# Kernel tuning notes

Measured on AMD Instinct MI355X. Metric: run time of the kernel, lower is better.

Reference implementation:

```python
import jax, jax.numpy as jnp
import numpy as np

NUM_HEADS = 8
TOP_K = 2
ROUTER_EPS = 1e-5
LN_EPS = 1e-5
ROPE_BASE = 10000.0


def _layernorm(x, g, b):
    m = x.mean(-1, keepdims=True)
    v = ((x - m) ** 2).mean(-1, keepdims=True)
    return (x - m) * jax.lax.rsqrt(v + LN_EPS) * g + b


def _rope_tables(frames, height, width, head_dim, dtype):
    # dim split per axis; head_dim divisible by 3 with even parts (96 -> 32/32/32)
    dpa = head_dim // 3

    def freqs(n, d):
        inv = 1.0 / (ROPE_BASE ** (jnp.arange(0, d, 2, dtype=jnp.float32) / d))
        f = jnp.outer(jnp.arange(n, dtype=jnp.float32), inv)
        return jnp.concatenate([f, f], axis=-1)  # [n, d]

    fx, fy, ft = freqs(width, dpa), freqs(height, dpa), freqs(frames, dpa)

    def grid(ax, ay, at):
        gx = jnp.broadcast_to(ax[None, None, :, :], (frames, height, width, dpa))
        gy = jnp.broadcast_to(ay[None, :, None, :], (frames, height, width, dpa))
        gt = jnp.broadcast_to(at[:, None, None, :], (frames, height, width, dpa))
        return jnp.concatenate([gx, gy, gt], -1).reshape(frames * height * width, 3 * dpa)

    cos = grid(jnp.cos(fx), jnp.cos(fy), jnp.cos(ft)).astype(dtype)
    sin = grid(jnp.sin(fx), jnp.sin(fy), jnp.sin(ft)).astype(dtype)
    return cos, sin


def _apply_rope(x, cos, sin):
    # x: [B, H, S, hd]; cos/sin: [S, hd] (broadcast over B, H)
    h = x.shape[-1] // 2
    rot = jnp.concatenate([-x[..., h:], x[..., :h]], axis=-1)
    return x * cos + rot * sin


def _expert(x, g, u, d):
    # SwiGLU expert: down(silu(gate(x)) * up(x))
    return (jax.nn.silu(x @ g) * (x @ u)) @ d


def _block(x, cos, sin, ln1_g, ln1_b, w_qkv, w_out, gate_w,
           eg, eu, ed, sg, su, sd, ln2_g, ln2_b):
    B, S, D = x.shape
    hd = D // NUM_HEADS
    # --- 3D-RoPE attention (pre-LN, non-causal) ---
    xn = _layernorm(x, ln1_g, ln1_b)
    qkv = (xn @ w_qkv).reshape(B, S, 3, NUM_HEADS, hd)
    q = jnp.moveaxis(qkv[:, :, 0], 1, 2)  # [B, H, S, hd]
    k = jnp.moveaxis(qkv[:, :, 1], 1, 2)
    v = jnp.moveaxis(qkv[:, :, 2], 1, 2)
    q = _apply_rope(q, cos, sin)
    k = _apply_rope(k, cos, sin)
    scores = jnp.einsum('bhqd,bhkd->bhqk', q, k) * (hd ** -0.5)
    attn = jax.nn.softmax(scores, axis=-1)
    o = jnp.einsum('bhqk,bhkd->bhqd', attn, v)
    o = jnp.moveaxis(o, 1, 2).reshape(B, S, D) @ w_out
    x = x + o
    # --- temporal MoE (top-k routing + shared expert) ---
    xf = x.reshape(-1, D)
    probs = jax.nn.softmax(xf @ gate_w, axis=-1)
    topv, topi = jax.lax.top_k(probs, TOP_K)
    topv = topv / (topv.sum(-1, keepdims=True) + ROUTER_EPS)
    E = eg.shape[0]
    # combine weight per (token, expert): sum over k slots routed to that expert
    comb = jnp.sum(topv[..., None] * (topi[..., None] == jnp.arange(E)), axis=1)  # [N, E]
    out = _expert(xf, sg, su, sd)  # shared expert on all tokens
    for e in range(E):
        out = out + comb[:, e:e + 1] * _expert(xf, eg[e], eu[e], ed[e])
    return _layernorm(x + out.reshape(B, S, D), ln2_g, ln2_b)


def setup_inputs() -> dict:
    key = jax.random.key(0)
    ks = jax.random.split(key, 10)
    B, S, D, F, E, L = 2, 2048, 768, 3072, 4, 2
    s = 0.02
    return {
        'x': jax.random.normal(ks[0], (B, S, D), jnp.float32),
        'height': 16, 'width': 16, 'frames': 8,
        'ln1_g': jnp.ones((L, D), jnp.float32),
        'ln1_b': jnp.zeros((L, D), jnp.float32),
        'w_qkv': jax.random.normal(ks[1], (L, D, 3 * D), jnp.float32) * s,
        'w_out': jax.random.normal(ks[2], (L, D, D), jnp.float32) * s,
        'gate_w': jax.random.normal(ks[3], (L, D, E), jnp.float32) * 0.01,
        'eg': jax.random.normal(ks[4], (L, E, D, F), jnp.float32) * s,
        'eu': jax.random.normal(ks[5], (L, E, D, F), jnp.float32) * s,
        'ed': jax.random.normal(ks[6], (L, E, F, D), jnp.float32) * s,
        'sg': jax.random.normal(ks[7], (L, D, F), jnp.float32) * s,
        'su': jax.random.normal(ks[8], (L, D, F), jnp.float32) * s,
        'sd': jax.random.normal(ks[9], (L, F, D), jnp.float32) * s,
        'ln2_g': jnp.ones((L, D), jnp.float32),
        'ln2_b': jnp.zeros((L, D), jnp.float32),
    }


def reference(x, height, width, frames, ln1_g, ln1_b, w_qkv, w_out, gate_w,
              eg, eu, ed, sg, su, sd, ln2_g, ln2_b):
    hd = x.shape[-1] // NUM_HEADS
    cos, sin = _rope_tables(frames, height, width, hd, x.dtype)
    for i in range(ln1_g.shape[0]):
        x = _block(x, cos, sin, ln1_g[i], ln1_b[i], w_qkv[i], w_out[i], gate_w[i],
                   eg[i], eu[i], ed[i], sg[i], su[i], sd[i], ln2_g[i], ln2_b[i])
    return x
```

## Files before the change

### kernel.cpp

```cpp
#include <hip/hip_runtime.h>
#include <stdint.h>

#define S_LEN 2048
#define DM    768
#define NHEAD 8
#define HDIM  96
#define HDP   128
#define FF    3072
#define FF2   6144
#define NEXP  4
#define NTOK  4096
#define NBH   16

typedef unsigned short u16;
typedef short bf16x8 __attribute__((ext_vector_type(8)));
typedef float f32x4 __attribute__((ext_vector_type(4)));
typedef __attribute__((address_space(1))) void* gptr_t;
typedef __attribute__((address_space(3))) void* lptr_t;

__device__ __forceinline__ u16 f2bf(float f) {
  union { float f; uint32_t u; } v; v.f = f;
  uint32_t r = v.u + 0x7FFFu + ((v.u >> 16) & 1u);
  return (u16)(r >> 16);
}
__device__ __forceinline__ float bf2f(u16 h) {
  union { uint32_t u; float f; } v; v.u = ((uint32_t)h) << 16;
  return v.f;
}
__device__ __forceinline__ void split2(float f, u16& hi, u16& lo) {
  u16 h = f2bf(f);
  lo = f2bf(f - bf2f(h));
  hi = h;
}
__device__ __forceinline__ float siluf(float g) {
  return g / (1.0f + expf(-g));
}
__device__ __forceinline__ void gload16(const void* g, void* l) {
  __builtin_amdgcn_global_load_lds((gptr_t)(void*)g, (lptr_t)l, 16, 0, 0);
}

template<int MODE>
__global__ __launch_bounds__(256) void gemm_nt(
    const u16* __restrict__ A, const u16* __restrict__ B, void* __restrict__ Cv,
    int M, int N, int K, int lda, int ldb, long sA, long sB, long sC, int kspl,
    u16* __restrict__ hb)
{
  __shared__ u16 As[2][128 * 32];
  __shared__ u16 Bs[2][128 * 32];
  const int z = blockIdx.z;
  const int bh = z / kspl;
  const int kc = z - bh * kspl;
  const u16* Az = A + (long)bh * sA;
  const u16* Bz = B + (long)bh * sB;
  const int brow = blockIdx.y << 7;
  const int bcol = blockIdx.x << 7;
  const int tid = threadIdx.x;
  const int wid = tid >> 6;
  const int lane = tid & 63;
  const int wr = (wid >> 1) << 6;
  const int wc = (wid & 1) << 6;

  f32x4 acc[4][4] = {};
  const int a0 = (wid << 11) + (lane << 4);

  auto stage = [&](int buf, int k0) {
#pragma unroll
    for (int c = 0; c < 2; ++c) {
      int ab = a0 + (c << 10);
      int row = ab >> 6;
      int kcol = (ab & 63) >> 1;
      int ld = (wid << 11) + (c << 10);
      gload16(Az + (long)(brow + row) * lda + (k0 + kcol), (char*)As[buf] + ld);
      gload16(Bz + (long)(bcol + row) * ldb + (k0 + kcol), (char*)Bs[buf] + ld);
    }
  };

  const int kt = K / kspl;
  const int kbeg = kc * kt;
  const int nt = kt >> 5;
  stage(0, kbeg);
  __syncthreads();
  for (int t = 0; t < nt; ++t) {
    const int cur = t & 1;
    if (t + 1 < nt) stage(cur ^ 1, kbeg + ((t + 1) << 5));
    bf16x8 af[4], bfr[4];
    const int lr = lane & 15;
    const int lk = (lane >> 4) << 4;
#pragma unroll
    for (int m = 0; m < 4; ++m)
      af[m] = *(const bf16x8*)((const char*)As[cur] + (((wr + m * 16 + lr) << 6) + lk));
#pragma unroll
    for (int n = 0; n < 4; ++n)
      bfr[n] = *(const bf16x8*)((const char*)Bs[cur] + (((wc + n * 16 + lr) << 6) + lk));
#pragma unroll
    for (int m = 0; m < 4; ++m)
// ... 71 lines not shown
      int kcol = (ab & 63) >> 1;
      long ao = (long)(brow + row) * lda + (k0 + kcol);
      long bo = (long)(bcol + row) * ldb + (k0 + kcol);
      int ld = (wid << 11) + (c << 10);
      gload16(Azh + ao, (char*)Ash[buf] + ld);
      gload16(Azl + ao, (char*)Asl[buf] + ld);
      gload16(Bzh + bo, (char*)Bsh[buf] + ld);
      gload16(Bzl + bo, (char*)Bsl[buf] + ld);
    }
  };

  const int kt = K / kspl;
  const int kbeg = kc * kt;
  const int nt = kt >> 5;
  stage(0, kbeg);
  __syncthreads();
  for (int t = 0; t < nt; ++t) {
    const int cur = t & 1;
    if (t + 1 < nt) stage(cur ^ 1, kbeg + ((t + 1) << 5));
    const int lr = lane & 15;
    const int lk = (lane >> 4) << 4;
    bf16x8 ah[4], al[4], bh_[4], bl[4];
#pragma unroll
    for (int m = 0; m < 4; ++m) {
      int off = ((wr + m * 16 + lr) << 6) + lk;
      ah[m] = *(const bf16x8*)((const char*)Ash[cur] + off);
      al[m] = *(const bf16x8*)((const char*)Asl[cur] + off);
    }
#pragma unroll
    for (int n = 0; n < 4; ++n) {
      int off = ((wc + n * 16 + lr) << 6) + lk;
      bh_[n] = *(const bf16x8*)((const char*)Bsh[cur] + off);
      bl[n] = *(const bf16x8*)((const char*)Bsl[cur] + off);
    }
#pragma unroll
    for (int m = 0; m < 4; ++m)
#pragma unroll
      for (int n = 0; n < 4; ++n) {
        acc[m][n] = __builtin_amdgcn_mfma_f32_16x16x32_bf16(al[m], bh_[n], acc[m][n], 0, 0, 0);
        acc[m][n] = __builtin_amdgcn_mfma_f32_16x16x32_bf16(ah[m], bl[n], acc[m][n], 0, 0, 0);
        acc[m][n] = __builtin_amdgcn_mfma_f32_16x16x32_bf16(ah[m], bh_[n], acc[m][n], 0, 0, 0);
      }
    if (t + 1 < nt) __syncthreads();
  }

  const int crow0 = brow + wr + ((lane >> 4) << 2);
  const int ccol0 = bcol + wc + (lane & 15);
  const long cbase = (long)bh * sC;
  if constexpr (MODE == 5) {
    const int pbase = (bcol + wc) >> 5;
#pragma unroll
    for (int m = 0; m < 4; ++m)
#pragma unroll
      for (int np = 0; np < 2; ++np)
#pragma unroll
        for (int j = 0; j < 4; ++j) {
          int r = crow0 + m * 16 + j;
          float g = acc[m][2 * np][j], u = acc[m][2 * np + 1][j];
          float h = siluf(g) * u;
          int hcol = ((pbase + np) << 4) + (lane & 15);
          u16 hh, ll; split2(h, hh, ll);
          hbh[(long)r * FF + hcol] = hh;
          hbl[(long)r * FF + hcol] = ll;
        }
  } else {
#pragma unroll
    for (int m = 0; m < 4; ++m)
#pragma unroll
      for (int n = 0; n < 4; ++n)
#pragma unroll
        for (int j = 0; j < 4; ++j) {
          long idx = cbase + (long)(crow0 + m * 16 + j) * N + (ccol0 + n * 16);
          if constexpr (MODE == 3) unsafeAtomicAdd(&C[idx], acc[m][n][j]);
          else C[idx] = acc[m][n][j];
        }
  }
}

template<int MODE>
__global__ __launch_bounds__(256) void gemm3i_nt(
    const u16* __restrict__ Ah, const u16* __restrict__ Al,
    const u16* __restrict__ Bh, const u16* __restrict__ Bl,
    float* __restrict__ C, int N, int K, int lda, int ldb, int ldc,
    const int* __restrict__ perm, const int* __restrict__ cntp,
    int kspl, u16* __restrict__ hbh, u16* __restrict__ hbl,
    const float* __restrict__ comb, int eidx)
{
  const int cn = *cntp;
  const int brow = blockIdx.y << 7;
  if (brow >= cn) return;
  __shared__ u16 Ash[2][128 * 32], Asl[2][128 * 32];
  __shared__ u16 Bsh[2][128 * 32], Bsl[2][128 * 32];
  const int kc = blockIdx.z;
  const int bcol = blockIdx.x << 7;
  const int tid = threadIdx.x;
  const int wid = tid >> 6;
  const int lane = tid & 63;
  const int wr = (wid >> 1) << 6;
  const int wc = (wid & 1) << 6;

  f32x4 acc[4][4] = {};
  const int a0 = (wid << 11) + (lane << 4);

  int arow[2];
#pragma unroll
  for (int c = 0; c < 2; ++c) {
    int ab = a0 + (c << 10);
    int row = ab >> 6;
    if constexpr (MODE == 5) {
      int g = brow + row;
      arow[c] = (g < cn) ? perm[g] : perm[brow];
    } else {
      arow[c] = brow + row;
    }
  }

  auto stage = [&](int buf, int k0) {
#pragma unroll
    for (int c = 0; c < 2; ++c) {
      int ab = a0 + (c << 10);
      int row = ab >> 6;
      int kcol = (ab & 63) >> 1;
      int ld = (wid << 11) + (c << 10);
      gload16(Ah + (long)arow[c] * lda + (k0 + kcol), (char*)Ash[buf] + ld);
      gload16(Al + (long)arow[c] * lda + (k0 + kcol), (char*)Asl[buf] + ld);
      long bo = (long)(bcol + row) * ldb + (k0 + kcol);
      gload16(Bh + bo, (char*)Bsh[buf] + ld);
      gload16(Bl + bo, (char*)Bsl[buf] + ld);
    }
  };

  const int kt = K / kspl;
  const int kbeg = kc * kt;
  const int nt = kt >> 5;
  stage(0, kbeg);
  __syncthreads();
  for (int t = 0; t < nt; ++t) {
    const int cur = t & 1;
    if (t + 1 < nt) stage(cur ^ 1, kbeg + ((t + 1) << 5));
    const int lr = lane & 15;
    const int lk = (lane >> 4) << 4;
    bf16x8 ah[4], al[4], bh_[4], bl[4];
#pragma unroll
    for (int m = 0; m < 4; ++m) {
      int off = ((wr + m * 16 + lr) << 6) + lk;
      ah[m] = *(const bf16x8*)((const char*)Ash[cur] + off);
      al[m] = *(const bf16x8*)((const char*)Asl[cur] + off);
    }
#pragma unroll
    for (int n = 0; n < 4; ++n) {
      int off = ((wc + n * 16 + lr) << 6) + lk;
      bh_[n] = *(const bf16x8*)((const char*)Bsh[cur] + off);
      bl[n] = *(const bf16x8*)((const char*)Bsl[cur] + off);
    }
#pragma unroll
    for (int m = 0; m < 4; ++m)
#pragma unroll
      for (int n = 0; n < 4; ++n) {
        acc[m][n] = __builtin_amdgcn_mfma_f32_16x16x32_bf16(al[m], bh_[n], acc[m][n], 0, 0, 0);
        acc[m][n] = __builtin_amdgcn_mfma_f32_16x16x32_bf16(ah[m], bl[n], acc[m][n], 0, 0, 0);
        acc[m][n] = __builtin_amdgcn_mfma_f32_16x16x32_bf16(ah[m], bh_[n], acc[m][n], 0, 0, 0);
      }
    if (t + 1 < nt) __syncthreads();
  }

  const int crow0 = brow + wr + ((lane >> 4) << 2);
  const int ccol0 = bcol + wc + (lane & 15);
  if constexpr (MODE == 5) {
    const int pbase = (bcol + wc) >> 5;
#pragma unroll
    for (int m = 0; m < 4; ++m)
#pragma unroll
      for (int j = 0; j < 4; ++j) {
        int r = crow0 + m * 16 + j;
        if (r < cn) {
          float w = comb[perm[r] * 4 + eidx];
#pragma unroll
          for (int np = 0; np < 2; ++np) {
            float g = acc[m][2 * np][j], u = acc[m][2 * np + 1][j];
            float h = siluf(g) * u * w;
            int hcol = ((pbase + np) << 4) + (lane & 15);
            u16 hh, ll; split2(h, hh, ll);
            hbh[(long)r * FF + hcol] = hh;
            hbl[(long)r * FF + hcol] = ll;
          }
        }
      }
  } else {
#pragma unroll
    for (int m = 0; m < 4; ++m)
#pragma unroll
      for (int n = 0; n < 4; ++n)
#pragma unroll
        for (int j = 0; j < 4; ++j) {
          int r = crow0 + m * 16 + j;
          if (r < cn) {
            int col = ccol0 + n * 16;
            unsafeAtomicAdd(&C[(long)perm[r] * ldc + col], acc[m][n][j]);
          }
        }
  }
}

template<int MODE>
__global__ __launch_bounds__(256) void gemmi_nt(
    const u16* __restrict__ A, const u16* __restrict__ B, void* __restrict__ Cv,
    int N, int K, int lda, int ldb, int ldc,
    const int* __restrict__ perm, const int* __restrict__ cntp,
    int kspl, u16* __restrict__ hb, const float* __restrict__ comb, int eidx)
{
  const int cn = *cntp;
  const int brow = blockIdx.y << 7;
  if (brow >= cn) return;
  __shared__ u16 As[2][128 * 32];
  __shared__ u16 Bs[2][128 * 32];
  const int kc = blockIdx.z;
  const int bcol = blockIdx.x << 7;
  const int tid = threadIdx.x;
  const int wid = tid >> 6;
  const int lane = tid & 63;
  const int wr = (wid >> 1) << 6;
  const int wc = (wid & 1) << 6;

  f32x4 acc[4][4] = {};
  const int a0 = (wid << 11) + (lane << 4);

  int arow[2];
#pragma unroll
  for (int c = 0; c < 2; ++c) {
    int ab = a0 + (c << 10);
    int row = ab >> 6;
    if constexpr (MODE == 5) {
      int g = brow + row;
      arow[c] = (g < cn) ? perm[g] : perm[brow];
    } else {
      arow[c] = brow + row;
    }
  }

  auto stage = [&](int buf, int k0) {
#pragma unroll
    for (int c = 0; c < 2; ++c) {
      int ab = a0 + (c << 10);
      int row = ab >> 6;
      int kcol = (ab & 63) >> 1;
      int ld = (wid << 11) + (c << 10);
      gload16(A + (long)arow[c] * lda + (k0 + kcol), (char*)As[buf] + ld);
      gload16(B + (long)(bcol + row) * ldb + (k0 + kcol), (char*)Bs[buf] + ld);
    }
  };

  const int kt = K / kspl;
  const int kbeg = kc * kt;
  const int nt = kt >> 5;
  stage(0, kbeg);
  __syncthreads();
  for (int t = 0; t < nt; ++t) {
    const int cur = t & 1;
    if (t + 1 < nt) stage(cur ^ 1, kbeg + ((t + 1) << 5));
    bf16x8 af[4], bfr[4];
    const int lr = lane & 15;
    const int lk = (lane >> 4) << 4;
#pragma unroll
    for (int m = 0; m < 4; ++m)
      af[m] = *(const bf16x8*)((const char*)As[cur] + (((wr + m * 16 + lr) << 6) + lk));
#pragma unroll
    for (int n = 0; n < 4; ++n)
      bfr[n] = *(const bf16x8*)((const char*)Bs[cur] + (((wc + n * 16 + lr) << 6) + lk));
#pragma unroll
    for (int m = 0; m < 4; ++m)
#pragma unroll
      for (int n = 0; n < 4; ++n)
        acc[m][n] = __builtin_amdgcn_mfma_f32_16x16x32_bf16(af[m], bfr[n], acc[m][n], 0, 0, 0);
    if (t + 1 < nt) __syncthreads();
  }

  const int crow0 = brow + wr + ((lane >> 4) << 2);
  const int ccol0 = bcol + wc + (lane & 15);
  if constexpr (MODE == 5) {
    const int pbase = (bcol + wc) >> 5;
#pragma unroll
    for (int m = 0; m < 4; ++m)
#pragma unroll
      for (int j = 0; j < 4; ++j) {
        int r = crow0 + m * 16 + j;
        if (r < cn) {
          float w = comb[perm[r] * 4 + eidx];
#pragma unroll
          for (int np = 0; np < 2; ++np) {
            float g = acc[m][2 * np][j], u = acc[m][2 * np + 1][j];
            int hcol = ((pbase + np) << 4) + (lane & 15);
            hb[(long)r * FF + hcol] = f2bf(siluf(g) * u * w);
          }
        }
      }
  } else {
#pragma unroll
    for (int m = 0; m < 4; ++m)
#pragma unroll
      for (int n = 0; n < 4; ++n)
#pragma unroll
        for (int j = 0; j < 4; ++j) {
          int r = crow0 + m * 16 + j;
          if (r < cn) {
            int col = ccol0 + n * 16;
            unsafeAtomicAdd((float*)Cv + (long)perm[r] * ldc + col, acc[m][n][j]);
          }
        }
  }
}

__global__ __launch_bounds__(256, 2) void fattn_k(
    const u16* __restrict__ qh, const u16* __restrict__ ql,
    const u16* __restrict__ kh, const u16* __restrict__ kl,
    const u16* __restrict__ vth, const u16* __restrict__ vtl,
    u16* __restrict__ omh, u16* __restrict__ oml, float scale)
{
  __shared__ u16 Ksh[64 * 128], Ksl[64 * 128];
  __shared__ u16 Vsh[128 * 64], Vsl[128 * 64];
  const int bh = blockIdx.x;
  const int qt = blockIdx.y;
  const int tid = threadIdx.x, wid = tid >> 6, lane = tid & 63;
  const int lr = lane & 15, lg = lane >> 4;
  const int q0 = qt * 64 + wid * 16;
  const long bhoff = (long)bh * S_LEN * HDP;
  const u16* Qh = qh + bhoff;  const u16* Ql = ql + bhoff;
  const u16* Kgh = kh + bhoff; const u16* Kgl = kl + bhoff;
  const u16* Vgh = vth + bhoff; const u16* Vgl = vtl + bhoff;

  bf16x8 qfh[4], qfl[4];
#pragma unroll
  for (int kk = 0; kk < 4; ++kk) {
    long o = (long)(q0 + lr) * HDP + kk * 32 + lg * 8;
    qfh[kk] = *(const bf16x8*)(Qh + o);
    qfl[kk] = *(const bf16x8*)(Ql + o);
  }

  f32x4 oacc[6] = {};
  float rm[4], rls[4];
#pragma unroll
  for (int j = 0; j < 4; ++j) { rm[j] = -1e30f; rls[j] = 0.f; }

  for (int t = 0; t < S_LEN / 64; ++t) {
    __syncthreads();
#pragma unroll
    for (int c = 0; c < 4; ++c) {
      int off = (tid + (c << 8)) << 4;
      {
        int lb = off ^ ((((off >> 8) & 7)) << 4);
        int row = lb >> 8, colh = (lb & 255) >> 1;
        long src = (long)(t * 64 + row) * HDP + colh;
        gload16(Kgh + src, (char*)Ksh + off);
        gload16(Kgl + src, (char*)Ksl + off);
      }
      {
        int lb = off ^ ((((off >> 7) & 7)) << 4);
        int row = lb >> 7, colh = (lb & 127) >> 1;
        long src = (long)row * S_LEN + t * 64 + colh;
        gload16(Vgh + src, (char*)Vsh + off);
        gload16(Vgl + src, (char*)Vsl + off);
      }
    }
    __syncthreads();

    f32x4 sacc[4] = {};
#pragma unroll
    for (int kk = 0; kk < 4; ++kk) {
      bf16x8 kbh[4], kbl[4];
#pragma unroll
      for (int n = 0; n < 4; ++n) {
        int byte = ((n * 16 + lr) << 8) + (kk << 6) + (lg << 4);
        byte ^= ((byte >> 8) & 7) << 4;
        kbh[n] = *(const bf16x8*)((const char*)Ksh + byte);
        kbl[n] = *(const bf16x8*)((const char*)Ksl + byte);
      }
      __builtin_amdgcn_s_setprio(1);
#pragma unroll
      for (int n = 0; n < 4; ++n) {
        sacc[n] = __builtin_amdgcn_mfma_f32_16x16x32_bf16(qfl[kk], kbh[n], sacc[n], 0, 0, 0);
        sacc[n] = __builtin_amdgcn_mfma_f32_16x16x32_bf16(qfh[kk], kbl[n], sacc[n], 0, 0, 0);
        sacc[n] = __builtin_amdgcn_mfma_f32_16x16x32_bf16(qfh[kk], kbh[n], sacc[n], 0, 0, 0);
      }
      __builtin_amdgcn_s_setprio(0);
    }
    __syncthreads();

#pragma unroll
    for (int j = 0; j < 4; ++j) {
      float mx = fmaxf(fmaxf(sacc[0][j], sacc[1][j]),
                       fmaxf(sacc[2][j], sacc[3][j])) * scale;
      mx = fmaxf(mx, __shfl_xor(mx, 1));
      mx = fmaxf(mx, __shfl_xor(mx, 2));
      mx = fmaxf(mx, __shfl_xor(mx, 4));
      mx = fmaxf(mx, __shfl_xor(mx, 8));
      float mnew = fmaxf(rm[j], mx);
      float corr = __expf(rm[j] - mnew);
      rm[j] = mnew;
      float ps = 0.f;
#pragma unroll
      for (int n = 0; n < 4; ++n) {
        float p = __expf(sacc[n][j] * scale - mnew);
        sacc[n][j] = p; ps += p;
      }
      ps += __shfl_xor(ps, 1); ps += __shfl_xor(ps, 2);
      ps += __shfl_xor(ps, 4); ps += __shfl_xor(ps, 8);
      rls[j] = rls[j] * corr + ps;
#pragma unroll
      for (int n2 = 0; n2 < 6; ++n2) oacc[n2][j] *= corr;
    }

    char* Pwh = (char*)Ksh + (wid << 11);
    char* Pwl = (char*)Ksl + (wid << 11);
#pragma unroll
    for (int n = 0; n < 4; ++n)
#pragma unroll
      for (int j = 0; j < 4; ++j) {
        int row = lg * 4 + j;
        int byte = (row << 7) + ((n * 16 + lr) << 1);
        byte ^= ((byte >> 7) & 7) << 4;
        u16 h, l; split2(sacc[n][j], h, l);
        *(u16*)(Pwh + byte) = h;
        *(u16*)(Pwl + byte) = l;
      }
    bf16x8 pah[2], pal[2];
#pragma unroll
    for (int kk = 0; kk < 2; ++kk) {
      int byte = (lr << 7) + (kk << 6) + (lg << 4);
      byte ^= ((byte >> 7) & 7) << 4;
      pah[kk] = *(const bf16x8*)(Pwh + byte);
      pal[kk] = *(const bf16x8*)(Pwl + byte);
    }

#pragma unroll
    for (int kk = 0; kk < 2; ++kk) {
      bf16x8 vbh[6], vbl[6];
#pragma unroll
      for (int n2 = 0; n2 < 6; ++n2) {
        int byte = ((n2 * 16 + lr) << 7) + (kk << 6) + (lg << 4);
        byte ^= ((byte >> 7) & 7) << 4;
        vbh[n2] = *(const bf16x8*)((const char*)Vsh + byte);
        vbl[n2] = *(const bf16x8*)((const char*)Vsl + byte);
      }
      __builtin_amdgcn_s_setprio(1);
#pragma unroll
      for (int n2 = 0; n2 < 6; ++n2) {
        oacc[n2] = __builtin_amdgcn_mfma_f32_16x16x32_bf16(pal[kk], vbh[n2], oacc[n2], 0, 0, 0);
        oacc[n2] = __builtin_amdgcn_mfma_f32_16x16x32_bf16(pah[kk], vbl[n2], oacc[n2], 0, 0, 0);
        oacc[n2] = __builtin_amdgcn_mfma_f32_16x16x32_bf16(pah[kk], vbh[n2], oacc[n2], 0, 0, 0);
      }
      __builtin_amdgcn_s_setprio(0);
    }
  }

  const int b = bh >> 3, h = bh & 7;
#pragma unroll
  for (int j = 0; j < 4; ++j) {
    float inv = 1.0f / rls[j];
    int q = q0 + lg * 4 + j;
    long base = ((long)(b * S_LEN + q)) * DM + h * HDIM;
#pragma unroll
    for (int n2 = 0; n2 < 6; ++n2) {
      int d = n2 * 16 + lr;
      u16 hh, ll; split2(oacc[n2][j] * inv, hh, ll);
      omh[base + d] = hh; oml[base + d] = ll;
    }
  }
}

__global__ void wconv_t(const float* __restrict__ in, u16* __restrict__ outh,
                        u16* __restrict__ outl, int R, int C, int ilv) {
  __shared__ float tile[32][33];
  int c0 = blockIdx.x << 5, r0 = blockIdx.y << 5;
  int tx = threadIdx.x;
  for (int rr = threadIdx.y; rr < 32; rr += 8)
    tile[rr][tx] = in[(long)(r0 + rr) * C + (c0 + tx)];
  __syncthreads();
  for (int rr = threadIdx.y; rr < 32; rr += 8) {
    u16 h, l; split2(tile[tx][rr], h, l);
    int f = c0 + rr;
    long orow = (ilv < 0) ? f : (((f >> 4) << 5) + (ilv << 4) + (f & 15));
    long o = orow * R + (r0 + tx);
    outh[o] = h; outl[o] = l;
  }
}

__global__ __launch_bounds__(256) void ln_k(const float* __restrict__ in,
    const float* __restrict__ g, const float* __restrict__ b,
    float* __restrict__ outf, u16* __restrict__ outh, u16* __restrict__ outl) {
  int row = blockIdx.x;
  const float* x = in + (long)row * DM;
  int tid = threadIdx.x;
  float v[3], s = 0.f, ss = 0.f;
#pragma unroll
  for (int i = 0; i < 3; ++i) { v[i] = x[tid + (i << 8)]; s += v[i]; ss += v[i] * v[i]; }
  __shared__ float red[2][4];
  for (int o = 32; o; o >>= 1) { s += __shfl_down(s, o); ss += __shfl_down(ss, o); }
  int wid = tid >> 6, lane = tid & 63;
  if (!lane) { red[0][wid] = s; red[1][wid] = ss; }
  __syncthreads();
  s = red[0][0] + red[0][1] + red[0][2] + red[0][3];
  ss = red[1][0] + red[1][1] + red[1][2] + red[1][3];
  float mean = s * (1.f / DM);
  float var = ss * (1.f / DM) - mean * mean;
  float rs = rsqrtf(var + 1e-5f);
#pragma unroll
  for (int i = 0; i < 3; ++i) {
    int c = tid + (i << 8);
    float y = (v[i] - mean) * rs * g[c] + b[c];
    if (outf) outf[(long)row * DM + c] = y;
    if (outh) { u16 h, l; split2(y, h, l); outh[(long)row * DM + c] = h; outl[(long)row * DM + c] = l; }
  }
}

__global__ void rope_tables_k(float* __restrict__ cosT, float* __restrict__ sinT) {
  int s = blockIdx.x, d = threadIdx.x;
  int xc = s & 15, y = (s >> 4) & 15, t = s >> 8;
  int axis = d / 32, fi = d & 15;
  int coord = axis == 0 ? xc : (axis == 1 ? y : t);
  float inv = powf(10000.0f, -(float)fi / 16.0f);
  float ang = (float)coord * inv;
  cosT[s * HDIM + d] = cosf(ang);
  sinT[s * HDIM + d] = sinf(ang);
}

__global__ __launch_bounds__(256) void rope_apply_k(const float* __restrict__ qkv,
    const float* __restrict__ cosT, const float* __restrict__ sinT,
    u16* __restrict__ qh, u16* __restrict__ ql,
    u16* __restrict__ kh, u16* __restrict__ kl) {
  int bs = blockIdx.x;
  int b = bs >> 11, s = bs & 2047;
  const float* base = qkv + ((long)(b * S_LEN + s) * 3) * DM;
  for (int idx = threadIdx.x; idx < DM; idx += 256) {
    int h = idx / HDIM, d = idx - h * HDIM;
    float c = cosT[s * HDIM + d], sn = sinT[s * HDIM + d];
    int pair = (d < 48) ? idx + 48 : idx - 48;
    float qv = base[idx], kv = base[DM + idx];
    float qr = (d < 48) ? -base[pair] : base[pair];
    float kr = (d < 48) ? -base[DM + pair] : base[DM + pair];
    long o = ((long)(b * NHEAD + h) * S_LEN + s) * HDP + d;
    u16 hh, ll;
    split2(qv * c + qr * sn, hh, ll); qh[o] = hh; ql[o] = ll;
    split2(kv * c + kr * sn, hh, ll); kh[o] = hh; kl[o] = ll;
  }
  int t = threadIdx.x;
  int h = t >> 5, d = HDIM + (t & 31);
  long o = ((long)(b * NHEAD + h) * S_LEN + s) * HDP + d;
  qh[o] = 0; ql[o] = 0; kh[o] = 0; kl[o] = 0;
}

__global__ void v_transpose_k(const float* __restrict__ qkv,
                              u16* __restrict__ vh, u16* __restrict__ vl) {
  __shared__ float tile[32][33];
  int bh = blockIdx.z, b = bh >> 3, h = bh & 7;
  int s0 = blockIdx.x << 5, d0 = blockIdx.y << 5;
  int tx = threadIdx.x;
  for (int r = threadIdx.y; r < 32; r += 8) {
    int s = s0 + r, d = d0 + tx;
    float v = 0.f;
    if (d < HDIM) v = qkv[((long)(b * S_LEN + s) * 3 + 2) * DM + h * HDIM + d];
    tile[r][tx] = v;
  }
  __syncthreads();
  for (int r = threadIdx.y; r < 32; r += 8) {
    int d = d0 + r;
    u16 hh, ll; split2(tile[tx][r], hh, ll);
    long o = ((long)bh * HDP + d) * S_LEN + (s0 + tx);
    vh[o] = hh; vl[o] = ll;
  }
}

__global__ __launch_bounds__(256) void router_k(const float* __restrict__ x,
    const float* __restrict__ gw, float* __restrict__ comb, int* __restrict__ mask) {
  int tok = blockIdx.x * 4 + (threadIdx.x >> 6);
  int lane = threadIdx.x & 63;
  const float* xr = x + (long)tok * DM;
  float a0 = 0, a1 = 0, a2 = 0, a3 = 0;
  for (int i = lane; i < DM; i += 64) {
    float xv = xr[i];
    const float* g = gw + i * 4;
    a0 += xv * g[0]; a1 += xv * g[1]; a2 += xv * g[2]; a3 += xv * g[3];
  }
  for (int o = 32; o; o >>= 1) {
    a0 += __shfl_down(a0, o); a1 += __shfl_down(a1, o);
    a2 += __shfl_down(a2, o); a3 += __shfl_down(a3, o);
  }
  if (lane == 0) {
    float p[4] = {a0, a1, a2, a3};
    float mx = fmaxf(fmaxf(p[0], p[1]), fmaxf(p[2], p[3]));
    float s = 0.f;
    for (int e = 0; e < 4; ++e) { p[e] = expf(p[e] - mx); s += p[e]; }
    for (int e = 0; e < 4; ++e) p[e] /= s;
    int i1 = 0;
    for (int e = 1; e < 4; ++e) if (p[e] > p[i1]) i1 = e;
    int i2 = -1;
    for (int e = 0; e < 4; ++e) if (e != i1 && (i2 < 0 || p[e] > p[i2])) i2 = e;
    float ssum = p[i1] + p[i2] + 1e-5f;
    float out[4] = {0, 0, 0, 0};
    out[i1] = p[i1] / ssum; out[i2] = p[i2] / ssum;
    for (int e = 0; e < 4; ++e) comb[tok * 4 + e] = out[e];
    mask[tok] = (1 << i1) | (1 << i2);
  }
}

__global__ void scan_k(const int* __restrict__ mask, int* __restrict__ perm,
                       int* __restrict__ cnt) {
  __shared__ int sd[256];
  __shared__ int base;
  int tid = threadIdx.x;
  int e = blockIdx.x;
  if (tid == 0) base = 0;
  __syncthreads();
  for (int c = 0; c < NTOK / 256; ++c) {
    int tok = c * 256 + tid;
    int f = (mask[tok] >> e) & 1;
    sd[tid] = f;
    __syncthreads();
    for (int s = 1; s < 256; s <<= 1) {
      int v = (tid >= s) ? sd[tid - s] : 0;
      __syncthreads();
      sd[tid] += v;
      __syncthreads();
    }
    if (f) perm[e * NTOK + base + sd[tid] - 1] = tok;
    int tot = sd[255];
    __syncthreads();
    if (tid == 0) base += tot;
    __syncthreads();
  }
  if (tid == 0) cnt[e] = base;
}

__global__ void f2b_k(const float* __restrict__ src, u16* __restrict__ dst, long n) {
  long i = (long)blockIdx.x * 256 + threadIdx.x;
  if (i < n) dst[i] = f2bf(src[i]);
}

__global__ void f2bsplit_k(const float* __restrict__ src, u16* __restrict__ dh,
                           u16* __restrict__ dl, long n) {
  long i = (long)blockIdx.x * 256 + threadIdx.x;
  if (i < n) { u16 h, l; split2(src[i], h, l); dh[i] = h; dl[i] = l; }
}

extern "C" void kernel_launch(void* const* d_in, const int* in_sizes, int n_in,
                              void* d_out, int out_size, void* d_ws, size_t ws_size,
                              hipStream_t stream) {
  (void)in_sizes; (void)n_in; (void)out_size; (void)ws_size;
  const float* x_in  = (const float*)d_in[0];
  const float* ln1_g = (const float*)d_in[4];
  const float* ln1_b = (const float*)d_in[5];
  const float* w_qkv = (const float*)d_in[6];
  const float* w_out = (const float*)d_in[7];
  const float* gatew = (const float*)d_in[8];
  const float* eg    = (const float*)d_in[9];
  const float* eu    = (const float*)d_in[10];
  const float* ed    = (const float*)d_in[11];
  const float* sg    = (const float*)d_in[12];
  const float* su    = (const float*)d_in[13];
  const float* sd    = (const float*)d_in[14];
  const float* ln2_g = (const float*)d_in[15];
  const float* ln2_b = (const float*)d_in[16];

  float* xc = (float*)d_out;
  char* W = (char*)d_ws;
  size_t off = 0;
  auto alloc = [&](size_t bytes) {
    size_t o = off; off = (off + bytes + 255) & ~(size_t)255; return o;
  };
  size_t o_cos  = alloc((size_t)S_LEN * HDIM * 4);
  size_t o_sin  = alloc((size_t)S_LEN * HDIM * 4);
  size_t o_xnh  = alloc((size_t)NTOK * DM * 2);
  size_t o_xnl  = alloc((size_t)NTOK * DM * 2);
  size_t o_qkv  = alloc((size_t)NTOK * 3 * DM * 4);
  size_t o_qph  = alloc((size_t)NBH * S_LEN * HDP * 2);
  size_t o_qpl  = alloc((size_t)NBH * S_LEN * HDP * 2);
  size_t o_kph  = alloc((size_t)NBH * S_LEN * HDP * 2);
  size_t o_kpl  = alloc((size_t)NBH * S_LEN * HDP * 2);
  size_t o_vth  = alloc((size_t)NBH * HDP * S_LEN * 2);
  size_t o_vtl  = alloc((size_t)NBH * HDP * S_LEN * 2);
  size_t o_omh  = alloc((size_t)NTOK * DM * 2);
  size_t o_oml  = alloc((size_t)NTOK * DM * 2);
  size_t o_comb = alloc((size_t)NTOK * 4 * 4);
  size_t o_mask = alloc((size_t)NTOK * 4);
  size_t o_perm = alloc((size_t)NEXP * NTOK * 4);
  size_t o_cnt  = alloc(256);
  size_t o_wqh  = alloc((size_t)3 * DM * DM * 2);
  size_t o_wql  = alloc((size_t)3 * DM * DM * 2);
  size_t o_woh  = alloc((size_t)DM * DM * 2);
  size_t o_wol  = alloc((size_t)DM * DM * 2);
  size_t o_sguh = alloc((size_t)FF2 * DM * 2);
  size_t o_sgul = alloc((size_t)FF2 * DM * 2);
  size_t o_sdh  = alloc((size_t)DM * FF * 2);
  size_t o_sdl  = alloc((size_t)DM * FF * 2);
  size_t o_eguh = alloc((size_t)FF2 * DM * 2);
  size_t o_egul = alloc((size_t)FF2 * DM * 2);
  size_t o_edh  = alloc((size_t)DM * FF * 2);
  size_t o_edl  = alloc((size_t)DM * FF * 2);
  size_t o_hbh  = alloc((size_t)NTOK * FF * 2);
  size_t o_hbl  = alloc((size_t)NTOK * FF * 2);

  float* cosT = (float*)(W + o_cos);
  float* sinT = (float*)(W + o_sin);
  u16*   xnh  = (u16*)(W + o_xnh);
  u16*   xnl  = (u16*)(W + o_xnl);
  float* qkv  = (float*)(W + o_qkv);
  u16 *qph = (u16*)(W + o_qph), *qpl = (u16*)(W + o_qpl);
  u16 *kph = (u16*)(W + o_kph), *kpl = (u16*)(W + o_kpl);
  u16 *vth = (u16*)(W + o_vth), *vtl = (u16*)(W + o_vtl);
  u16 *omh = (u16*)(W + o_omh), *oml = (u16*)(W + o_oml);
  float* comb = (float*)(W + o_comb);
  int* maskb  = (int*)(W + o_mask);
  int* permb  = (int*)(W + o_perm);
  int* cntb   = (int*)(W + o_cnt);
  u16 *wqh = (u16*)(W + o_wqh), *wql = (u16*)(W + o_wql);
  u16 *woh = (u16*)(W + o_woh), *wol = (u16*)(W + o_wol);
  u16 *sguh = (u16*)(W + o_sguh), *sgul = (u16*)(W + o_sgul);
  u16 *sdh = (u16*)(W + o_sdh), *sdl = (u16*)(W + o_sdl);
  u16 *eguh = (u16*)(W + o_eguh), *egul = (u16*)(W + o_egul);
  u16 *edh = (u16*)(W + o_edh), *edl = (u16*)(W + o_edl);
  u16 *hbh = (u16*)(W + o_hbh), *hbl = (u16*)(W + o_hbl);

  const long ND = (long)NTOK * DM;
  const int gND = (int)((ND + 255) / 256);

  hipMemcpyAsync(xc, x_in, (size_t)ND * 4, hipMemcpyDeviceToDevice, stream);
  rope_tables_k<<<S_LEN, HDIM, 0, stream>>>(cosT, sinT);

  dim3 tb(32, 8, 1);
  for (int l = 0; l < 2; ++l) {
    const float* wqkv_l = w_qkv + (size_t)l * DM * 3 * DM;
    const float* wout_l = w_out + (size_t)l * DM * DM;
    const float* gw_l   = gatew + (size_t)l * DM * 4;
    const float* eg_l = eg + (size_t)l * NEXP * DM * FF;
    const float* eu_l = eu + (size_t)l * NEXP * DM * FF;
    const float* ed_l = ed + (size_t)l * NEXP * FF * DM;
    const float* sg_l = sg + (size_t)l * DM * FF;
    const float* su_l = su + (size_t)l * DM * FF;
    const float* sd_l = sd + (size_t)l * FF * DM;

    wconv_t<<<dim3(3 * DM / 32, DM / 32), tb, 0, stream>>>(wqkv_l, wqh, wql, DM, 3 * DM, -1);
    wconv_t<<<dim3(DM / 32, DM / 32), tb, 0, stream>>>(wout_l, woh, wol, DM, DM, -1);
    wconv_t<<<dim3(FF / 32, DM / 32), tb, 0, stream>>>(sg_l, sguh, sgul, DM, FF, 0);
    wconv_t<<<dim3(FF / 32, DM / 32), tb, 0, stream>>>(su_l, sguh, sgul, DM, FF, 1);
    wconv_t<<<dim3(DM / 32, FF / 32), tb, 0, stream>>>(sd_l, sdh, sdl, FF, DM, -1);

    ln_k<<<NTOK, 256, 0, stream>>>(xc, ln1_g + l * DM, ln1_b + l * DM, nullptr, xnh, xnl);
    gemm3_nt<0><<<dim3(3 * DM >> 7, NTOK >> 7, 1), 256, 0, stream>>>(
        xnh, xnl, wqh, wql, qkv, NTOK, 3 * DM, DM, DM, DM, 0, 0, 0, 1, nullptr, nullptr);
    rope_apply_k<<<NTOK, 256, 0, stream>>>(qkv, cosT, sinT, qph, qpl, kph, kpl);
    v_transpose_k<<<dim3(S_LEN / 32, HDP / 32, NBH), tb, 0, stream>>>(qkv, vth, vtl);
    fattn_k<<<dim3(NBH, S_LEN / 64), dim3(256), 0, stream>>>(
        qph, qpl, kph, kpl, vth, vtl, omh, oml, 0.10206207261596575f);
    gemm3_nt<3><<<dim3(DM >> 7, NTOK >> 7, 2), 256, 0, stream>>>(
        omh, oml, woh, wol, xc, NTOK, DM, DM, DM, DM, 0, 0, 0, 2, nullptr, nullptr);

    router_k<<<NTOK / 4, 256, 0, stream>>>(xc, gw_l, comb, maskb);
    scan_k<<<NEXP, 256, 0, stream>>>(maskb, permb, cntb);

    if (l == 0) {
      f2bsplit_k<<<gND, 256, 0, stream>>>(xc, xnh, xnl, ND);
      gemm3_nt<5><<<dim3(FF2 >> 7, NTOK >> 7, 1), 256, 0, stream>>>(
          xnh, xnl, sguh, sgul, nullptr, NTOK, FF2, DM, DM, DM, 0, 0, 0, 1, hbh, hbl);
      gemm3_nt<3><<<dim3(DM >> 7, NTOK >> 7, 4), 256, 0, stream>>>(
          hbh, hbl, sdh, sdl, xc, NTOK, DM, FF, FF, FF, 0, 0, 0, 4, nullptr, nullptr);
      for (int e = 0; e < NEXP; ++e) {
        wconv_t<<<dim3(FF / 32, DM / 32), tb, 0, stream>>>(eg_l + (size_t)e * DM * FF, eguh, egul, DM, FF, 0);
        wconv_t<<<dim3(FF / 32, DM / 32), tb, 0, stream>>>(eu_l + (size_t)e * DM * FF, eguh, egul, DM, FF, 1);
        wconv_t<<<dim3(DM / 32, FF / 32), tb, 0, stream>>>(ed_l + (size_t)e * FF * DM, edh, edl, FF, DM, -1);
        const int* pe = permb + e * NTOK;
        const int* ce = cntb + e;
        gemm3i_nt<5><<<dim3(FF2 >> 7, NTOK >> 7, 1), 256, 0, stream>>>(
            xnh, xnl, eguh, egul, nullptr, FF2, DM, DM, DM, FF2, pe, ce, 1, hbh, hbl, comb, e);
        gemm3i_nt<1><<<dim3(DM >> 7, NTOK >> 7, 4), 256, 0, stream>>>(
            hbh, hbl, edh, edl, xc, DM, FF, FF, FF, DM, pe, ce, 4, nullptr, nullptr, nullptr, e);
      }
    } else {
      f2b_k<<<gND, 256, 0, stream>>>(xc, xnh, ND);
      gemm_nt<5><<<dim3(FF2 >> 7, NTOK >> 7, 1), 256, 0, stream>>>(
          xnh, sguh, nullptr, NTOK, FF2, DM, DM, DM, 0, 0, 0, 1, hbh);
      gemm_nt<3><<<dim3(DM >> 7, NTOK >> 7, 4), 256, 0, stream>>>(
          hbh, sdh, xc, NTOK, DM, FF, FF, FF, 0, 0, 0, 4, nullptr);
      for (int e = 0; e < NEXP; ++e) {
        wconv_t<<<dim3(FF / 32, DM / 32), tb, 0, stream>>>(eg_l + (size_t)e * DM * FF, eguh, egul, DM, FF, 0);
        wconv_t<<<dim3(FF / 32, DM / 32), tb, 0, stream>>>(eu_l + (size_t)e * DM * FF, eguh, egul, DM, FF, 1);
        wconv_t<<<dim3(DM / 32, FF / 32), tb, 0, stream>>>(ed_l + (size_t)e * FF * DM, edh, edl, FF, DM, -1);
        const int* pe = permb + e * NTOK;
        const int* ce = cntb + e;
        gemmi_nt<5><<<dim3(FF2 >> 7, NTOK >> 7, 1), 256, 0, stream>>>(
            xnh, eguh, nullptr, FF2, DM, DM, DM, FF2, pe, ce, 1, hbh, comb, e);
        gemmi_nt<3><<<dim3(DM >> 7, NTOK >> 7, 4), 256, 0, stream>>>(
            hbh, edh, xc, DM, FF, FF, FF, DM, pe, ce, 4, nullptr, nullptr, e);
      }
    }
    ln_k<<<NTOK, 256, 0, stream>>>(xc, ln2_g + l * DM, ln2_b + l * DM, xc, nullptr, nullptr);
  }
}
```

Before: 2.140 ms.

## Batch all experts into single grouped GEMM launches with compacted hidden buffer

Replaces the per-expert loop of weight conversions and two GEMMs with grouped launches whose z-dimension indexes the expert (and K-split). Each expert's routed rows are written into a compacted hidden buffer at an offset computed by a new cbase kernel. Expert weights are converted for all experts at once, and the workspace is aliased so that attention scratch and expert weights share memory. This cuts launch count and the serialization of small, partly idle grids, at the cost of a reduced down-projection K-split and extra workspace aliasing complexity.

```diff
diff --git a/kernel.cpp b/kernel.cpp
--- a/kernel.cpp
+++ b/kernel.cpp
@@ -11,6 +11,7 @@
 #define NEXP  4
 #define NTOK  4096
 #define NBH   16
+#define HBROWS (2 * NTOK)
 
 typedef unsigned short u16;
 typedef short bf16x8 __attribute__((ext_vector_type(8)));
@@ -248,16 +249,22 @@
     const u16* __restrict__ Ah, const u16* __restrict__ Al,
     const u16* __restrict__ Bh, const u16* __restrict__ Bl,
     float* __restrict__ C, int N, int K, int lda, int ldb, int ldc,
-    const int* __restrict__ perm, const int* __restrict__ cntp,
-    int kspl, u16* __restrict__ hbh, u16* __restrict__ hbl,
-    const float* __restrict__ comb, int eidx)
+    const int* __restrict__ perm, const int* __restrict__ cnt,
+    const int* __restrict__ cbase, int kspl, long wstride,
+    u16* __restrict__ hbh, u16* __restrict__ hbl, const float* __restrict__ comb)
 {
-  const int cn = *cntp;
+  const int z = blockIdx.z;
+  const int e = z / kspl;
+  const int kc = z - e * kspl;
+  const int cn = cnt[e];
   const int brow = blockIdx.y << 7;
   if (brow >= cn) return;
+  const int cb = cbase[e];
+  const int* pe = perm + e * NTOK;
+  const u16* Bhe = Bh + (long)e * wstride;
+  const u16* Ble = Bl + (long)e * wstride;
   __shared__ u16 Ash[2][128 * 32], Asl[2][128 * 32];
   __shared__ u16 Bsh[2][128 * 32], Bsl[2][128 * 32];
-  const int kc = blockIdx.z;
   const int bcol = blockIdx.x << 7;
   const int tid = threadIdx.x;
   const int wid = tid >> 6;
@@ -273,11 +280,11 @@
   for (int c = 0; c < 2; ++c) {
     int ab = a0 + (c << 10);
     int row = ab >> 6;
+    int g = brow + row;
     if constexpr (MODE == 5) {
-      int g = brow + row;
-      arow[c] = (g < cn) ? perm[g] : perm[brow];
+      arow[c] = (g < cn) ? pe[g] : pe[brow];
     } else {
-      arow[c] = brow + row;
+      arow[c] = cb + ((g < cn) ? g : (cn - 1));
     }
   }
 
@@ -291,8 +298,8 @@
       gload16(Ah + (long)arow[c] * lda + (k0 + kcol), (char*)Ash[buf] + ld);
       gload16(Al + (long)arow[c] * lda + (k0 + kcol), (char*)Asl[buf] + ld);
       long bo = (long)(bcol + row) * ldb + (k0 + kcol);
-      gload16(Bh + bo, (char*)Bsh[buf] + ld);
-      gload16(Bl + bo, (char*)Bsl[buf] + ld);
+      gload16(Bhe + bo, (char*)Bsh[buf] + ld);
+      gload16(Ble + bo, (char*)Bsl[buf] + ld);
     }
   };
 
@@ -340,15 +347,15 @@
       for (int j = 0; j < 4; ++j) {
         int r = crow0 + m * 16 + j;
         if (r < cn) {
-          float w = comb[perm[r] * 4 + eidx];
+          float w = comb[pe[r] * 4 + e];
 #pragma unroll
           for (int np = 0; np < 2; ++np) {
             float g = acc[m][2 * np][j], u = acc[m][2 * np + 1][j];
             float h = siluf(g) * u * w;
             int hcol = ((pbase + np) << 4) + (lane & 15);
             u16 hh, ll; split2(h, hh, ll);
-            hbh[(long)r * FF + hcol] = hh;
-            hbl[(long)r * FF + hcol] = ll;
+            hbh[(long)(cb + r) * FF + hcol] = hh;
+            hbl[(long)(cb + r) * FF + hcol] = ll;
           }
         }
       }
@@ -362,7 +369,7 @@
           int r = crow0 + m * 16 + j;
           if (r < cn) {
             int col = ccol0 + n * 16;
-            unsafeAtomicAdd(&C[(long)perm[r] * ldc + col], acc[m][n][j]);
+            unsafeAtomicAdd(&C[(long)pe[r] * ldc + col], acc[m][n][j]);
           }
         }
   }
@@ -372,15 +379,21 @@
 __global__ __launch_bounds__(256) void gemmi_nt(
     const u16* __restrict__ A, const u16* __restrict__ B, void* __restrict__ Cv,
     int N, int K, int lda, int ldb, int ldc,
-    const int* __restrict__ perm, const int* __restrict__ cntp,
-    int kspl, u16* __restrict__ hb, const float* __restrict__ comb, int eidx)
+    const int* __restrict__ perm, const int* __restrict__ cnt,
+    const int* __restrict__ cbase, int kspl, long wstride,
+    u16* __restrict__ hb, const float* __restrict__ comb)
 {
-  const int cn = *cntp;
+  const int z = blockIdx.z;
+  const int e = z / kspl;
+  const int kc = z - e * kspl;
+  const int cn = cnt[e];
   const int brow = blockIdx.y << 7;
   if (brow >= cn) return;
+  const int cb = cbase[e];
+  const int* pe = perm + e * NTOK;
+  const u16* Be = B + (long)e * wstride;
   __shared__ u16 As[2][128 * 32];
   __shared__ u16 Bs[2][128 * 32];
-  const int kc = blockIdx.z;
   const int bcol = blockIdx.x << 7;
   const int tid = threadIdx.x;
   const int wid = tid >> 6;
@@ -396,11 +409,11 @@
   for (int c = 0; c < 2; ++c) {
     int ab = a0 + (c << 10);
     int row = ab >> 6;
+    int g = brow + row;
     if constexpr (MODE == 5) {
-      int g = brow + row;
-      arow[c] = (g < cn) ? perm[g] : perm[brow];
+      arow[c] = (g < cn) ? pe[g] : pe[brow];
     } else {
-      arow[c] = brow + row;
+      arow[c] = cb + ((g < cn) ? g : (cn - 1));
     }
   }
 
@@ -412,7 +425,7 @@
       int kcol = (ab & 63) >> 1;
       int ld = (wid << 11) + (c << 10);
       gload16(A + (long)arow[c] * lda + (k0 + kcol), (char*)As[buf] + ld);
-      gload16(B + (long)(bcol + row) * ldb + (k0 + kcol), (char*)Bs[buf] + ld);
+      gload16(Be + (long)(bcol + row) * ldb + (k0 + kcol), (char*)Bs[buf] + ld);
     }
   };
 
@@ -451,12 +464,12 @@
       for (int j = 0; j < 4; ++j) {
         int r = crow0 + m * 16 + j;
         if (r < cn) {
-          float w = comb[perm[r] * 4 + eidx];
+          float w = comb[pe[r] * 4 + e];
 #pragma unroll
           for (int np = 0; np < 2; ++np) {
             float g = acc[m][2 * np][j], u = acc[m][2 * np + 1][j];
             int hcol = ((pbase + np) << 4) + (lane & 15);
-            hb[(long)r * FF + hcol] = f2bf(siluf(g) * u * w);
+            hb[(long)(cb + r) * FF + hcol] = f2bf(siluf(g) * u * w);
           }
         }
       }
@@ -470,7 +483,7 @@
           int r = crow0 + m * 16 + j;
           if (r < cn) {
             int col = ccol0 + n * 16;
-            unsafeAtomicAdd((float*)Cv + (long)perm[r] * ldc + col, acc[m][n][j]);
+            unsafeAtomicAdd((float*)Cv + (long)pe[r] * ldc + col, acc[m][n][j]);
           }
         }
   }
@@ -634,8 +647,11 @@
 }
 
 __global__ void wconv_t(const float* __restrict__ in, u16* __restrict__ outh,
-                        u16* __restrict__ outl, int R, int C, int ilv) {
+                        u16* __restrict__ outl, int R, int C, int ilv,
+                        long inStride, long outStride) {
   __shared__ float tile[32][33];
+  long z = blockIdx.z;
+  in += z * inStride; outh += z * outStride; outl += z * outStride;
   int c0 = blockIdx.x << 5, r0 = blockIdx.y << 5;
   int tx = threadIdx.x;
   for (int rr = threadIdx.y; rr < 32; rr += 8)
@@ -796,6 +812,13 @@
   if (tid == 0) cnt[e] = base;
 }
 
+__global__ void cbase_k(const int* __restrict__ cnt, int* __restrict__ cbase) {
+  if (threadIdx.x == 0) {
+    int b = 0;
+    for (int e = 0; e < NEXP; ++e) { cbase[e] = b; b += cnt[e]; }
+  }
+}
+
 __global__ void f2b_k(const float* __restrict__ src, u16* __restrict__ dst, long n) {
   long i = (long)blockIdx.x * 256 + threadIdx.x;
   if (i < n) dst[i] = f2bf(src[i]);
@@ -836,53 +859,62 @@
   size_t o_sin  = alloc((size_t)S_LEN * HDIM * 4);
   size_t o_xnh  = alloc((size_t)NTOK * DM * 2);
   size_t o_xnl  = alloc((size_t)NTOK * DM * 2);
-  size_t o_qkv  = alloc((size_t)NTOK * 3 * DM * 4);
-  size_t o_qph  = alloc((size_t)NBH * S_LEN * HDP * 2);
-  size_t o_qpl  = alloc((size_t)NBH * S_LEN * HDP * 2);
-  size_t o_kph  = alloc((size_t)NBH * S_LEN * HDP * 2);
-  size_t o_kpl  = alloc((size_t)NBH * S_LEN * HDP * 2);
-  size_t o_vth  = alloc((size_t)NBH * HDP * S_LEN * 2);
-  size_t o_vtl  = alloc((size_t)NBH * HDP * S_LEN * 2);
-  size_t o_omh  = alloc((size_t)NTOK * DM * 2);
-  size_t o_oml  = alloc((size_t)NTOK * DM * 2);
   size_t o_comb = alloc((size_t)NTOK * 4 * 4);
   size_t o_mask = alloc((size_t)NTOK * 4);
   size_t o_perm = alloc((size_t)NEXP * NTOK * 4);
   size_t o_cnt  = alloc(256);
-  size_t o_wqh  = alloc((size_t)3 * DM * DM * 2);
-  size_t o_wql  = alloc((size_t)3 * DM * DM * 2);
-  size_t o_woh  = alloc((size_t)DM * DM * 2);
-  size_t o_wol  = alloc((size_t)DM * DM * 2);
-  size_t o_sguh = alloc((size_t)FF2 * DM * 2);
-  size_t o_sgul = alloc((size_t)FF2 * DM * 2);
-  size_t o_sdh  = alloc((size_t)DM * FF * 2);
-  size_t o_sdl  = alloc((size_t)DM * FF * 2);
-  size_t o_eguh = alloc((size_t)FF2 * DM * 2);
-  size_t o_egul = alloc((size_t)FF2 * DM * 2);
-  size_t o_edh  = alloc((size_t)DM * FF * 2);
-  size_t o_edl  = alloc((size_t)DM * FF * 2);
-  size_t o_hbh  = alloc((size_t)NTOK * FF * 2);
-  size_t o_hbl  = alloc((size_t)NTOK * FF * 2);
+  size_t o_cb   = alloc(256);
+  const size_t EGU_B = (size_t)NEXP * FF2 * DM * 2;
+  const size_t SGU_B = (size_t)FF2 * DM * 2;
+  const size_t SD_B  = (size_t)DM * FF * 2;
+  const size_t A_BYTES = 2 * EGU_B + 2 * SGU_B + 2 * SD_B;
+  size_t oA = alloc(A_BYTES);
+  size_t o_qkv = oA;
+  size_t o_qph = oA + (size_t)NTOK * 3 * DM * 4;
+  size_t o_qpl = o_qph + (size_t)NBH * S_LEN * HDP * 2;
+  size_t o_kph = o_qpl + (size_t)NBH * S_LEN * HDP * 2;
+  size_t o_kpl = o_kph + (size_t)NBH * S_LEN * HDP * 2;
+  size_t o_vth = o_kpl + (size_t)NBH * S_LEN * HDP * 2;
+  size_t o_vtl = o_vth + (size_t)NBH * HDP * S_LEN * 2;
+  size_t o_omh = o_vtl + (size_t)NBH * HDP * S_LEN * 2;
+  size_t o_oml = o_omh + (size_t)NTOK * DM * 2;
+  size_t o_eguh = oA;
+  size_t o_egul = oA + EGU_B;
+  size_t o_sguh = oA + 2 * EGU_B;
+  size_t o_sgul = o_sguh + SGU_B;
+  size_t o_sdh  = o_sgul + SGU_B;
+  size_t o_sdl  = o_sdh + SD_B;
+  size_t o_edh  = oA;
+  size_t o_edl  = oA + (size_t)NEXP * DM * FF * 2;
+  const size_t H_BYTES = (size_t)2 * HBROWS * FF * 2;
+  size_t oH = alloc(H_BYTES);
+  size_t o_wqh = oH;
+  size_t o_wql = o_wqh + (size_t)3 * DM * DM * 2;
+  size_t o_woh = o_wql + (size_t)3 * DM * DM * 2;
+  size_t o_wol = o_woh + (size_t)DM * DM * 2;
+  size_t o_hbh = oH;
+  size_t o_hbl = oH + (size_t)HBROWS * FF * 2;
 
   float* cosT = (float*)(W + o_cos);
   float* sinT = (float*)(W + o_sin);
   u16*   xnh  = (u16*)(W + o_xnh);
   u16*   xnl  = (u16*)(W + o_xnl);
+  float* comb = (float*)(W + o_comb);
+  int* maskb  = (int*)(W + o_mask);
+  int* permb  = (int*)(W + o_perm);
+  int* cntb   = (int*)(W + o_cnt);
+  int* cbaseb = (int*)(W + o_cb);
   float* qkv  = (float*)(W + o_qkv);
   u16 *qph = (u16*)(W + o_qph), *qpl = (u16*)(W + o_qpl);
   u16 *kph = (u16*)(W + o_kph), *kpl = (u16*)(W + o_kpl);
   u16 *vth = (u16*)(W + o_vth), *vtl = (u16*)(W + o_vtl);
   u16 *omh = (u16*)(W + o_omh), *oml = (u16*)(W + o_oml);
-  float* comb = (float*)(W + o_comb);
-  int* maskb  = (int*)(W + o_mask);
-  int* permb  = (int*)(W + o_perm);
-  int* cntb   = (int*)(W + o_cnt);
+  u16 *eguh = (u16*)(W + o_eguh), *egul = (u16*)(W + o_egul);
+  u16 *sguh = (u16*)(W + o_sguh), *sgul = (u16*)(W + o_sgul);
+  u16 *sdh = (u16*)(W + o_sdh), *sdl = (u16*)(W + o_sdl);
+  u16 *edh = (u16*)(W + o_edh), *edl = (u16*)(W + o_edl);
   u16 *wqh = (u16*)(W + o_wqh), *wql = (u16*)(W + o_wql);
   u16 *woh = (u16*)(W + o_woh), *wol = (u16*)(W + o_wol);
-  u16 *sguh = (u16*)(W + o_sguh), *sgul = (u16*)(W + o_sgul);
-  u16 *sdh = (u16*)(W + o_sdh), *sdl = (u16*)(W + o_sdl);
-  u16 *eguh = (u16*)(W + o_eguh), *egul = (u16*)(W + o_egul);
-  u16 *edh = (u16*)(W + o_edh), *edl = (u16*)(W + o_edl);
   u16 *hbh = (u16*)(W + o_hbh), *hbl = (u16*)(W + o_hbl);
 
   const long ND = (long)NTOK * DM;
@@ -903,11 +935,8 @@
     const float* su_l = su + (size_t)l * DM * FF;
     const float* sd_l = sd + (size_t)l * FF * DM;
 
-    wconv_t<<<dim3(3 * DM / 32, DM / 32), tb, 0, stream>>>(wqkv_l, wqh, wql, DM, 3 * DM, -1);
-    wconv_t<<<dim3(DM / 32, DM / 32), tb, 0, stream>>>(wout_l, woh, wol, DM, DM, -1);
-    wconv_t<<<dim3(FF / 32, DM / 32), tb, 0, stream>>>(sg_l, sguh, sgul, DM, FF, 0);
-    wconv_t<<<dim3(FF / 32, DM / 32), tb, 0, stream>>>(su_l, sguh, sgul, DM, FF, 1);
-    wconv_t<<<dim3(DM / 32, FF / 32), tb, 0, stream>>>(sd_l, sdh, sdl, FF, DM, -1);
+    wconv_t<<<dim3(3 * DM / 32, DM / 32, 1), tb, 0, stream>>>(wqkv_l, wqh, wql, DM, 3 * DM, -1, 0, 0);
+    wconv_t<<<dim3(DM / 32, DM / 32, 1), tb, 0, stream>>>(wout_l, woh, wol, DM, DM, -1, 0, 0);
 
     ln_k<<<NTOK, 256, 0, stream>>>(xc, ln1_g + l * DM, ln1_b + l * DM, nullptr, xnh, xnl);
     gemm3_nt<0><<<dim3(3 * DM >> 7, NTOK >> 7, 1), 256, 0, stream>>>(
@@ -921,6 +950,15 @@
 
     router_k<<<NTOK / 4, 256, 0, stream>>>(xc, gw_l, comb, maskb);
     scan_k<<<NEXP, 256, 0, stream>>>(maskb, permb, cntb);
+    cbase_k<<<1, 64, 0, stream>>>(cntb, cbaseb);
+
+    wconv_t<<<dim3(FF / 32, DM / 32, 1), tb, 0, stream>>>(sg_l, sguh, sgul, DM, FF, 0, 0, 0);
+    wconv_t<<<dim3(FF / 32, DM / 32, 1), tb, 0, stream>>>(su_l, sguh, sgul, DM, FF, 1, 0, 0);
+    wconv_t<<<dim3(DM / 32, FF / 32, 1), tb, 0, stream>>>(sd_l, sdh, sdl, FF, DM, -1, 0, 0);
+    wconv_t<<<dim3(FF / 32, DM / 32, NEXP), tb, 0, stream>>>(
+        eg_l, eguh, egul, DM, FF, 0, (long)DM * FF, (long)FF2 * DM);
+    wconv_t<<<dim3(FF / 32, DM / 32, NEXP), tb, 0, stream>>>(
+        eu_l, eguh, egul, DM, FF, 1, (long)DM * FF, (long)FF2 * DM);
 
     if (l == 0) {
       f2bsplit_k<<<gND, 256, 0, stream>>>(xc, xnh, xnl, ND);
@@ -928,34 +966,28 @@
           xnh, xnl, sguh, sgul, nullptr, NTOK, FF2, DM, DM, DM, 0, 0, 0, 1, hbh, hbl);
       gemm3_nt<3><<<dim3(DM >> 7, NTOK >> 7, 4), 256, 0, stream>>>(
           hbh, hbl, sdh, sdl, xc, NTOK, DM, FF, FF, FF, 0, 0, 0, 4, nullptr, nullptr);
-      for (int e = 0; e < NEXP; ++e) {
-        wconv_t<<<dim3(FF / 32, DM / 32), tb, 0, stream>>>(eg_l + (size_t)e * DM * FF, eguh, egul, DM, FF, 0);
-        wconv_t<<<dim3(FF / 32, DM / 32), tb, 0, stream>>>(eu_l + (size_t)e * DM * FF, eguh, egul, DM, FF, 1);
-        wconv_t<<<dim3(DM / 32, FF / 32), tb, 0, stream>>>(ed_l + (size_t)e * FF * DM, edh, edl, FF, DM, -1);
-        const int* pe = permb + e * NTOK;
-        const int* ce = cntb + e;
-        gemm3i_nt<5><<<dim3(FF2 >> 7, NTOK >> 7, 1), 256, 0, stream>>>(
-            xnh, xnl, eguh, egul, nullptr, FF2, DM, DM, DM, FF2, pe, ce, 1, hbh, hbl, comb, e);
-        gemm3i_nt<1><<<dim3(DM >> 7, NTOK >> 7, 4), 256, 0, stream>>>(
-            hbh, hbl, edh, edl, xc, DM, FF, FF, FF, DM, pe, ce, 4, nullptr, nullptr, nullptr, e);
-      }
+      gemm3i_nt<5><<<dim3(FF2 >> 7, NTOK >> 7, NEXP), 256, 0, stream>>>(
+          xnh, xnl, eguh, egul, nullptr, FF2, DM, DM, DM, FF2,
+          permb, cntb, cbaseb, 1, (long)FF2 * DM, hbh, hbl, comb);
+      wconv_t<<<dim3(DM / 32, FF / 32, NEXP), tb, 0, stream>>>(
+          ed_l, edh, edl, FF, DM, -1, (long)FF * DM, (long)DM * FF);
+      gemm3i_nt<1><<<dim3(DM >> 7, NTOK >> 7, NEXP * 2), 256, 0, stream>>>(
+          hbh, hbl, edh, edl, xc, DM, FF, FF, FF, DM,
+          permb, cntb, cbaseb, 2, (long)DM * FF, nullptr, nullptr, nullptr);
     } else {
       f2b_k<<<gND, 256, 0, stream>>>(xc, xnh, ND);
       gemm_nt<5><<<dim3(FF2 >> 7, NTOK >> 7, 1), 256, 0, stream>>>(
           xnh, sguh, nullptr, NTOK, FF2, DM, DM, DM, 0, 0, 0, 1, hbh);
       gemm_nt<3><<<dim3(DM >> 7, NTOK >> 7, 4), 256, 0, stream>>>(
           hbh, sdh, xc, NTOK, DM, FF, FF, FF, 0, 0, 0, 4, nullptr);
-      for (int e = 0; e < NEXP; ++e) {
-        wconv_t<<<dim3(FF / 32, DM / 32), tb, 0, stream>>>(eg_l + (size_t)e * DM * FF, eguh, egul, DM, FF, 0);
-        wconv_t<<<dim3(FF / 32, DM / 32), tb, 0, stream>>>(eu_l + (size_t)e * DM * FF, eguh, egul, DM, FF, 1);
-        wconv_t<<<dim3(DM / 32, FF / 32), tb, 0, stream>>>(ed_l + (size_t)e * FF * DM, edh, edl, FF, DM, -1);
-        const int* pe = permb + e * NTOK;
-        const int* ce = cntb + e;
-        gemmi_nt<5><<<dim3(FF2 >> 7, NTOK >> 7, 1), 256, 0, stream>>>(
-            xnh, eguh, nullptr, FF2, DM, DM, DM, FF2, pe, ce, 1, hbh, comb, e);
-        gemmi_nt<3><<<dim3(DM >> 7, NTOK >> 7, 4), 256, 0, stream>>>(
-            hbh, edh, xc, DM, FF, FF, FF, DM, pe, ce, 4, nullptr, nullptr, e);
-      }
+      gemmi_nt<5><<<dim3(FF2 >> 7, NTOK >> 7, NEXP), 256, 0, stream>>>(
+          xnh, eguh, nullptr, FF2, DM, DM, DM, FF2,
+          permb, cntb, cbaseb, 1, (long)FF2 * DM, hbh, comb);
+      wconv_t<<<dim3(DM / 32, FF / 32, NEXP), tb, 0, stream>>>(
+          ed_l, edh, edl, FF, DM, -1, (long)FF * DM, (long)DM * FF);
+      gemmi_nt<3><<<dim3(DM >> 7, NTOK >> 7, NEXP * 2), 256, 0, stream>>>(
+          hbh, edh, xc, DM, FF, FF, FF, DM,
+          permb, cntb, cbaseb, 2, (long)DM * FF, nullptr, nullptr);
     }
     ln_k<<<NTOK, 256, 0, stream>>>(xc, ln2_g + l * DM, ln2_b + l * DM, xc, nullptr, nullptr);
   }
```

New measurement: 1.860 ms. -13.1%, faster.
